# Performance work log

Hardware: AMD Instinct MI355X
Metric: run time of the kernel (lower is better)

The kernel has to match this reference:

```python
import jax, jax.numpy as jnp
import numpy as np

B, N, DIM = 8, 16384, 256
DIM_HEAD, NUM_HEADS = 64, 8
D = DIM_HEAD * NUM_HEADS  # 512
SCALE = DIM_HEAD ** (-0.5)


def setup_inputs() -> dict:
    key = jax.random.key(0)
    ks = jax.random.split(key, 11)
    s = 0.02
    return {
        "x": jax.random.normal(ks[0], (B, N, DIM), dtype=jnp.float32),
        "Wq": jax.random.normal(ks[1], (DIM, D), dtype=jnp.float32) * s,
        "bq": jax.random.normal(ks[2], (D,), dtype=jnp.float32) * s,
        "Wk": jax.random.normal(ks[3], (DIM, D), dtype=jnp.float32) * s,
        "bk": jax.random.normal(ks[4], (D,), dtype=jnp.float32) * s,
        "qw": jax.random.normal(ks[5], (D, 1), dtype=jnp.float32),  # query_weight parameter
        "Wp": jax.random.normal(ks[6], (D, D), dtype=jnp.float32) * s,
        "bp": jax.random.normal(ks[7], (D,), dtype=jnp.float32) * s,
        "Wo": jax.random.normal(ks[8], (D, DIM_HEAD), dtype=jnp.float32) * s,
        "bo": jax.random.normal(ks[9], (DIM_HEAD,), dtype=jnp.float32) * s,
    }


def reference(x, Wq, bq, Wk, bk, qw, Wp, bp, Wo, bo):
    # query, key: [B, N, D]
    query = jnp.einsum("bnc,cd->bnd", x, Wq) + bq
    key = jnp.einsum("bnc,cd->bnd", x, Wk) + bk
    # per-token scalar score: [B, N, 1]
    score = (query @ qw) * SCALE
    # global attention context: sum over sequence axis -> [B, 1, D]
    attn_weight = jnp.sum(score * query, axis=1, keepdims=True)
    # broadcast (repeat over N), gate keys, project, residual add of query
    out = jnp.einsum("bnd,de->bne", attn_weight * key, Wp) + bp + query
    # output projection D -> dim_head: [B, N, DIM_HEAD]
    out = jnp.einsum("bnd,dh->bnh", out, Wo) + bo
    return out
```

## Files before the change

kernel.cpp:

```cpp
#include <hip/hip_runtime.h>
#include <hip/hip_bf16.h>


#define NN 16384
#define CC 256
#define DD 512
#define HH 64
#define SCALE_F 0.125f

#define OFF_SX    0
#define OFF_TSUM  2048
#define OFF_WQQ   2056
#define OFF_BQQ   2312
#define OFF_WPWO  2320
#define OFF_WQWO  35088
#define OFF_CBIAS 51472
#define OFF_BEFF  51536
#define OFF_WEFFT 52048
#define OFF_AW    117584

typedef unsigned short ushort_t;
typedef __attribute__((ext_vector_type(8))) short short8;
typedef __attribute__((ext_vector_type(4))) float floatx4;

__device__ __forceinline__ unsigned short f2bf(float f) {
    __hip_bfloat16 h = __float2bfloat16(f);
    return __builtin_bit_cast(unsigned short, h);
}

__global__ __launch_bounds__(256) void k_prep(
    const float* __restrict__ Wq, const float* __restrict__ bq,
    const float* __restrict__ qw, const float* __restrict__ Wp,
    const float* __restrict__ bp, const float* __restrict__ Wo,
    const float* __restrict__ bo, float* __restrict__ ws)
{
    __shared__ float lds[2056];
    const int tid = threadIdx.x;
    const int bid = blockIdx.x;

    if (bid < 128) {
        const int d0 = bid * 4;
        for (int i = tid; i < 2048; i += 256) lds[i] = Wp[d0 * 512 + i];
        __syncthreads();
        const int dl = tid >> 6, h = tid & 63;
        float acc = 0.f;
        for (int e = 0; e < 512; ++e)
            acc = fmaf(lds[dl * 512 + e], Wo[e * 64 + h], acc);
        ws[OFF_WPWO + (d0 + dl) * 64 + h] = acc;
    } else if (bid < 192) {
        const int c0 = (bid - 128) * 4;
        for (int i = tid; i < 2048; i += 256) lds[i] = Wq[c0 * 512 + i];
        __syncthreads();
        const int cl = tid >> 6, h = tid & 63;
        float acc = 0.f;
        for (int e = 0; e < 512; ++e)
            acc = fmaf(lds[cl * 512 + e], Wo[e * 64 + h], acc);
        ws[OFF_WQWO + (c0 + cl) * 64 + h] = acc;
    } else if (bid == 192) {
        float* lb = lds + 2048;
        for (int i = tid; i < 512; i += 256) lds[i] = qw[i];
        if (tid == 0) *lb = 0.f;
        __syncthreads();
        const float* wr = Wq + tid * 512;
        float acc = 0.f;
        for (int d = 0; d < 512; ++d) acc = fmaf(wr[d], lds[d], acc);
        ws[OFF_WQQ + tid] = acc;
        float pb = fmaf(bq[tid], lds[tid], bq[tid + 256] * lds[tid + 256]);
#pragma unroll
        for (int m = 1; m < 64; m <<= 1) pb += __shfl_xor(pb, m);
        if ((tid & 63) == 0) atomicAdd(lb, pb);
        __syncthreads();
        if (tid == 0) ws[OFF_BQQ] = *lb;
    } else if (bid == 193) {
        const int h = tid & 63, part = tid >> 6;
        float acc = 0.f;
        for (int d = part * 128; d < part * 128 + 128; ++d)
            acc = fmaf(bq[d] + bp[d], Wo[d * 64 + h], acc);
        lds[part * 64 + h] = acc;
        __syncthreads();
        if (tid < 64)
            ws[OFF_CBIAS + tid] = bo[tid] + lds[tid] + lds[64 + tid] +
                                  lds[128 + tid] + lds[192 + tid];
    } else {
        for (int i = tid; i < 2056; i += 256) ws[OFF_SX + i] = 0.f;
    }
}

__global__ __launch_bounds__(256) void k_phase1(
    const float* __restrict__ x, float* __restrict__ ws)
{
    const int tid  = threadIdx.x;
    const int lane = tid & 63;
    const int wave = tid >> 6;
    const int quad = lane >> 4;
    const int l15  = lane & 15;
    __shared__ float lacc[256];
    __shared__ float ltsum;

    floatx4 wv[4];
#pragma unroll
    for (int j = 0; j < 4; ++j)
        wv[j] = *(const floatx4*)(ws + OFF_WQQ + j * 64 + l15 * 4);
    const float bqq = ws[OFF_BQQ];

    const int vb = blockIdx.x;
    const int b = vb >> 7;
    const int rbase = (vb & 127) * 128;
    lacc[tid] = 0.f;
    if (tid == 0) ltsum = 0.f;
    __syncthreads();

    const float* xb = x + (size_t)b * NN * CC;
    const int r0 = rbase + wave * 32 + quad;
    floatx4 accs[4];
#pragma unroll
    for (int j = 0; j < 4; ++j)
#pragma unroll
        for (int k = 0; k < 4; ++k) accs[j][k] = 0.f;
    float ts = 0.f;

#pragma unroll 2
    for (int it = 0; it < 8; ++it) {
        const float* xr = xb + (size_t)(r0 + it * 4) * CC + l15 * 4;
        const floatx4 x0 = *(const floatx4*)(xr);
        const floatx4 x1 = *(const floatx4*)(xr + 64);
        const floatx4 x2 = *(const floatx4*)(xr + 128);
        const floatx4 x3 = *(const floatx4*)(xr + 192);
        float p = 0.f;
#pragma unroll
        for (int k = 0; k < 4; ++k) {
            p = fmaf(x0[k], wv[0][k], p);
            p = fmaf(x1[k], wv[1][k], p);
            p = fmaf(x2[k], wv[2][k], p);
            p = fmaf(x3[k], wv[3][k], p);
        }
        p += __shfl_xor(p, 1);
        p += __shfl_xor(p, 2);
        p += __shfl_xor(p, 4);
        p += __shfl_xor(p, 8);
        const float t = SCALE_F * (p + bqq);
        ts += t;
#pragma unroll
        for (int k = 0; k < 4; ++k) {
            accs[0][k] = fmaf(t, x0[k], accs[0][k]);
            accs[1][k] = fmaf(t, x1[k], accs[1][k]);
            accs[2][k] = fmaf(t, x2[k], accs[2][k]);
            accs[3][k] = fmaf(t, x3[k], accs[3][k]);
        }
    }

#pragma unroll
    for (int j = 0; j < 4; ++j)
#pragma unroll
        for (int k = 0; k < 4; ++k) {
            float v = accs[j][k];
            v += __shfl_xor(v, 16);
            v += __shfl_xor(v, 32);
            if (quad == 0) atomicAdd(&lacc[j * 64 + l15 * 4 + k], v);
        }
    if (l15 == 0) atomicAdd(&ltsum, ts);
    __syncthreads();
    atomicAdd(&ws[OFF_SX + b * 256 + tid], lacc[tid]);
    if (tid == 0) atomicAdd(&ws[OFF_TSUM + b], ltsum);
}

__global__ __launch_bounds__(256) void k_aw(
    const float* __restrict__ Wq, const float* __restrict__ bq,
    float* __restrict__ ws)
{
    const int tid = threadIdx.x;
    const int b = blockIdx.y;
    const int d = blockIdx.x * 256 + tid;
    __shared__ float lsx[256];
    __shared__ float lts;
    lsx[tid] = ws[OFF_SX + b * 256 + tid];
    if (tid == 0) lts = ws[OFF_TSUM + b];
    __syncthreads();

    float a[8];
#pragma unroll
    for (int j = 0; j < 8; ++j) a[j] = 0.f;
    for (int c = 0; c < 256; c += 8) {
#pragma unroll
        for (int j = 0; j < 8; ++j)
            a[j] = fmaf(lsx[c + j], Wq[(c + j) * 512 + d], a[j]);
    }
    const float s = ((a[0] + a[1]) + (a[2] + a[3])) +
                    ((a[4] + a[5]) + (a[6] + a[7]));
    ws[OFF_AW + b * 512 + d] = lts * bq[d] + s;
}

__global__ __launch_bounds__(256) void k_weff(
    const float* __restrict__ Wk, const float* __restrict__ bk,
    float* __restrict__ ws)
{
    const int tid = threadIdx.x;
    const int b = blockIdx.y;
    const int c0 = blockIdx.x * 4;
    __shared__ float lred[256];

    const int cl = tid >> 6, h = tid & 63;
    const int c = c0 + cl;
    const float* law = ws + OFF_AW + (size_t)b * 512;
    const float* wkr = Wk + (size_t)c * 512;
    const float* wp  = ws + OFF_WPWO;

    float a0 = 0.f, a1 = 0.f, a2 = 0.f, a3 = 0.f;
    for (int d = 0; d < 512; d += 4) {
        a0 = fmaf(wkr[d + 0] * law[d + 0], wp[(d + 0) * 64 + h], a0);
        a1 = fmaf(wkr[d + 1] * law[d + 1], wp[(d + 1) * 64 + h], a1);
        a2 = fmaf(wkr[d + 2] * law[d + 2], wp[(d + 2) * 64 + h], a2);
        a3 = fmaf(wkr[d + 3] * law[d + 3], wp[(d + 3) * 64 + h], a3);
    }
    const float acc = ws[OFF_WQWO + c * 64 + h] + ((a0 + a1) + (a2 + a3));

    ushort_t* wt = (ushort_t*)(ws + OFF_WEFFT) + (size_t)b * (HH * CC);
    wt[(size_t)h * CC + c] = f2bf(acc);

    if (blockIdx.x == 0) {
        const int part = tid >> 6;
        float a = 0.f;
        for (int d = part * 128; d < part * 128 + 128; ++d)
            a = fmaf(bk[d] * law[d], wp[d * 64 + h], a);
        lred[tid] = a;
        __syncthreads();
        if (tid < 64)
            ws[OFF_BEFF + b * 64 + tid] = ws[OFF_CBIAS + tid] + lred[tid] +
                lred[64 + tid] + lred[128 + tid] + lred[192 + tid];
    }
}

__global__ __launch_bounds__(256) void k_out(
    const float* __restrict__ x, const float* __restrict__ ws,
    float* __restrict__ out)
{
    const int tid  = threadIdx.x;
    const int lane = tid & 63;
    const int wave = tid >> 6;
    const int quad = lane >> 4;
    const int l15  = lane & 15;
    __shared__ __align__(16) ushort_t lwt[64 * 264];

    const int vb = blockIdx.x;
    const int b = vb >> 7;
    const int rt0 = vb & 127;

    const int row0_0 = rt0 * 64 + wave * 16;
    const float* xr0 = x + ((size_t)b * NN + row0_0 + l15) * CC + quad * 8;
    short8 afrag0[8];
#pragma unroll
    for (int kk = 0; kk < 8; ++kk) {
        const floatx4 u0 = *(const floatx4*)(xr0 + kk * 32);
        const floatx4 u1 = *(const floatx4*)(xr0 + kk * 32 + 4);
        short8 t;
        t[0] = (short)f2bf(u0[0]); t[1] = (short)f2bf(u0[1]);
        t[2] = (short)f2bf(u0[2]); t[3] = (short)f2bf(u0[3]);
        t[4] = (short)f2bf(u1[0]); t[5] = (short)f2bf(u1[1]);
        t[6] = (short)f2bf(u1[2]); t[7] = (short)f2bf(u1[3]);
        afrag0[kk] = t;
    }

    const ushort_t* wt = (const ushort_t*)(ws + OFF_WEFFT) + (size_t)b * (HH * CC);
    for (int o = tid; o < 2048; o += 256) {
        const int h = o >> 5, seg = o & 31;
        *(short8*)(lwt + h * 264 + seg * 8) = *(const short8*)(wt + h * 256 + seg * 8);
    }
    __syncthreads();

    const float* beff = ws + OFF_BEFF + b * 64;
    float bias[4];
#pragma unroll
    for (int ht = 0; ht < 4; ++ht) bias[ht] = beff[ht * 16 + l15];

    {
        floatx4 acc[4];
#pragma unroll
        for (int ht = 0; ht < 4; ++ht)
#pragma unroll
            for (int r = 0; r < 4; ++r) acc[ht][r] = 0.f;
#pragma unroll
        for (int kk = 0; kk < 8; ++kk)
#pragma unroll
            for (int ht = 0; ht < 4; ++ht) {
                const short8 bf =
                    *(const short8*)(lwt + (ht * 16 + l15) * 264 + quad * 8 + kk * 32);
                acc[ht] = __builtin_amdgcn_mfma_f32_16x16x32_bf16(
                    afrag0[kk], bf, acc[ht], 0, 0, 0);
            }
#pragma unroll
        for (int ht = 0; ht < 4; ++ht) {
            const int h = ht * 16 + l15;
#pragma unroll
            for (int r = 0; r < 4; ++r) {
                const int row = row0_0 + quad * 4 + r;
                out[((size_t)b * NN + row) * HH + h] = acc[ht][r] + bias[ht];
            }
        }
    }

    {
        const int row0_1 = (rt0 + 128) * 64 + wave * 16;
        const float* xr1 = x + ((size_t)b * NN + row0_1 + l15) * CC + quad * 8;
        short8 afrag1[8];
#pragma unroll
        for (int kk = 0; kk < 8; ++kk) {
            const floatx4 u0 = *(const floatx4*)(xr1 + kk * 32);
            const floatx4 u1 = *(const floatx4*)(xr1 + kk * 32 + 4);
            short8 t;
            t[0] = (short)f2bf(u0[0]); t[1] = (short)f2bf(u0[1]);
            t[2] = (short)f2bf(u0[2]); t[3] = (short)f2bf(u0[3]);
            t[4] = (short)f2bf(u1[0]); t[5] = (short)f2bf(u1[1]);
            t[6] = (short)f2bf(u1[2]); t[7] = (short)f2bf(u1[3]);
            afrag1[kk] = t;
        }
        floatx4 acc[4];
#pragma unroll
        for (int ht = 0; ht < 4; ++ht)
#pragma unroll
            for (int r = 0; r < 4; ++r) acc[ht][r] = 0.f;
#pragma unroll
        for (int kk = 0; kk < 8; ++kk)
#pragma unroll
            for (int ht = 0; ht < 4; ++ht) {
                const short8 bf =
                    *(const short8*)(lwt + (ht * 16 + l15) * 264 + quad * 8 + kk * 32);
                acc[ht] = __builtin_amdgcn_mfma_f32_16x16x32_bf16(
                    afrag1[kk], bf, acc[ht], 0, 0, 0);
            }
#pragma unroll
        for (int ht = 0; ht < 4; ++ht) {
            const int h = ht * 16 + l15;
#pragma unroll
            for (int r = 0; r < 4; ++r) {
                const int row = row0_1 + quad * 4 + r;
                out[((size_t)b * NN + row) * HH + h] = acc[ht][r] + bias[ht];
            }
        }
    }
}

extern "C" void kernel_launch(void* const* d_in, const int* in_sizes, int n_in,
                              void* d_out, int out_size, void* d_ws, size_t ws_size,
                              hipStream_t stream) {
    const float* x  = (const float*)d_in[0];
    const float* Wq = (const float*)d_in[1];
    const float* bq = (const float*)d_in[2];
    const float* Wk = (const float*)d_in[3];
    const float* bk = (const float*)d_in[4];
    const float* qw = (const float*)d_in[5];
    const float* Wp = (const float*)d_in[6];
    const float* bp = (const float*)d_in[7];
    const float* Wo = (const float*)d_in[8];
    const float* bo = (const float*)d_in[9];
    float* ws  = (float*)d_ws;
    float* out = (float*)d_out;

    hipLaunchKernelGGL(k_prep,   dim3(195),    dim3(256), 0, stream,
                       Wq, bq, qw, Wp, bp, Wo, bo, ws);
    hipLaunchKernelGGL(k_phase1, dim3(1024),   dim3(256), 0, stream, x, ws);
    hipLaunchKernelGGL(k_aw,     dim3(2, 8),   dim3(256), 0, stream, Wq, bq, ws);
    hipLaunchKernelGGL(k_weff,   dim3(64, 8),  dim3(256), 0, stream, Wk, bk, ws);
    hipLaunchKernelGGL(k_out,    dim3(1024),   dim3(256), 0, stream, x, ws, out);
}
```

Baseline: 301.3 us.

## Split reductions across waves in small prep kernels to raise parallelism

The weight-folding kernels (prep, aw, weff) now split each dot-product reduction over four waves with an LDS reduction. Each block handles one output row instead of four, so the grids grow from 195/16/512 blocks to 770/64/2048. The goal is shorter serial reduction chains and more latency hiding in these small, latency-bound kernels. The cost is extra LDS reductions, barriers and more blocks launched; the main phase1 and out kernels are unchanged.

```diff
diff --git a/kernel.cpp b/kernel.cpp
--- a/kernel.cpp
+++ b/kernel.cpp
@@ -34,54 +34,61 @@
     const float* __restrict__ bp, const float* __restrict__ Wo,
     const float* __restrict__ bo, float* __restrict__ ws)
 {
-    __shared__ float lds[2056];
+    __shared__ float lds[520];
     const int tid = threadIdx.x;
     const int bid = blockIdx.x;
 
-    if (bid < 128) {
-        const int d0 = bid * 4;
-        for (int i = tid; i < 2048; i += 256) lds[i] = Wp[d0 * 512 + i];
-        __syncthreads();
-        const int dl = tid >> 6, h = tid & 63;
-        float acc = 0.f;
-        for (int e = 0; e < 512; ++e)
-            acc = fmaf(lds[dl * 512 + e], Wo[e * 64 + h], acc);
-        ws[OFF_WPWO + (d0 + dl) * 64 + h] = acc;
-    } else if (bid < 192) {
-        const int c0 = (bid - 128) * 4;
-        for (int i = tid; i < 2048; i += 256) lds[i] = Wq[c0 * 512 + i];
-        __syncthreads();
-        const int cl = tid >> 6, h = tid & 63;
-        float acc = 0.f;
-        for (int e = 0; e < 512; ++e)
-            acc = fmaf(lds[cl * 512 + e], Wo[e * 64 + h], acc);
-        ws[OFF_WQWO + (c0 + cl) * 64 + h] = acc;
-    } else if (bid == 192) {
-        float* lb = lds + 2048;
+    if (bid < 768) {
+        const bool is_wp = (bid < 512);
+        const int row = is_wp ? bid : (bid - 512);
+        const float* src = is_wp ? (Wp + (size_t)row * 512)
+                                 : (Wq + (size_t)row * 512);
+        const int h = tid & 63, part = tid >> 6;
+        const int e0 = part * 128;
+        float a0 = 0.f, a1 = 0.f, a2 = 0.f, a3 = 0.f;
+        for (int e = e0; e < e0 + 128; e += 4) {
+            a0 = fmaf(src[e + 0], Wo[(e + 0) * 64 + h], a0);
+            a1 = fmaf(src[e + 1], Wo[(e + 1) * 64 + h], a1);
+            a2 = fmaf(src[e + 2], Wo[(e + 2) * 64 + h], a2);
+            a3 = fmaf(src[e + 3], Wo[(e + 3) * 64 + h], a3);
+        }
+        lds[tid] = ((a0 + a1) + (a2 + a3));
+        __syncthreads();
+        if (tid < 64) {
+            const float v = lds[tid] + lds[64 + tid] + lds[128 + tid] + lds[192 + tid];
+            const int off = is_wp ? (OFF_WPWO + row * 64) : (OFF_WQWO + row * 64);
+            ws[off + tid] = v;
+        }
+    } else if (bid == 768) {
+        float* lb = lds + 512;
         for (int i = tid; i < 512; i += 256) lds[i] = qw[i];
         if (tid == 0) *lb = 0.f;
         __syncthreads();
-        const float* wr = Wq + tid * 512;
-        float acc = 0.f;
-        for (int d = 0; d < 512; ++d) acc = fmaf(wr[d], lds[d], acc);
-        ws[OFF_WQQ + tid] = acc;
+        const float* wr = Wq + (size_t)tid * 512;
+        float a0 = 0.f, a1 = 0.f, a2 = 0.f, a3 = 0.f;
+        for (int d = 0; d < 512; d += 4) {
+            a0 = fmaf(wr[d + 0], lds[d + 0], a0);
+            a1 = fmaf(wr[d + 1], lds[d + 1], a1);
+            a2 = fmaf(wr[d + 2], lds[d + 2], a2);
+            a3 = fmaf(wr[d + 3], lds[d + 3], a3);
+        }
+        ws[OFF_WQQ + tid] = ((a0 + a1) + (a2 + a3));
         float pb = fmaf(bq[tid], lds[tid], bq[tid + 256] * lds[tid + 256]);
 #pragma unroll
         for (int m = 1; m < 64; m <<= 1) pb += __shfl_xor(pb, m);
         if ((tid & 63) == 0) atomicAdd(lb, pb);
         __syncthreads();
         if (tid == 0) ws[OFF_BQQ] = *lb;
-    } else if (bid == 193) {
+    } else {
         const int h = tid & 63, part = tid >> 6;
         float acc = 0.f;
         for (int d = part * 128; d < part * 128 + 128; ++d)
             acc = fmaf(bq[d] + bp[d], Wo[d * 64 + h], acc);
-        lds[part * 64 + h] = acc;
+        lds[tid] = acc;
         __syncthreads();
         if (tid < 64)
             ws[OFF_CBIAS + tid] = bo[tid] + lds[tid] + lds[64 + tid] +
                                   lds[128 + tid] + lds[192 + tid];
-    } else {
         for (int i = tid; i < 2056; i += 256) ws[OFF_SX + i] = 0.f;
     }
 }
@@ -170,24 +177,30 @@
 {
     const int tid = threadIdx.x;
     const int b = blockIdx.y;
-    const int d = blockIdx.x * 256 + tid;
+    const int dl = tid & 63, part = tid >> 6;
+    const int d = blockIdx.x * 64 + dl;
     __shared__ float lsx[256];
+    __shared__ float lred[256];
     __shared__ float lts;
     lsx[tid] = ws[OFF_SX + b * 256 + tid];
     if (tid == 0) lts = ws[OFF_TSUM + b];
     __syncthreads();
 
-    float a[8];
-#pragma unroll
-    for (int j = 0; j < 8; ++j) a[j] = 0.f;
-    for (int c = 0; c < 256; c += 8) {
-#pragma unroll
-        for (int j = 0; j < 8; ++j)
-            a[j] = fmaf(lsx[c + j], Wq[(c + j) * 512 + d], a[j]);
-    }
-    const float s = ((a[0] + a[1]) + (a[2] + a[3])) +
-                    ((a[4] + a[5]) + (a[6] + a[7]));
-    ws[OFF_AW + b * 512 + d] = lts * bq[d] + s;
+    const int c0 = part * 64;
+    float a0 = 0.f, a1 = 0.f, a2 = 0.f, a3 = 0.f;
+    for (int c = c0; c < c0 + 64; c += 4) {
+        a0 = fmaf(lsx[c + 0], Wq[(c + 0) * 512 + d], a0);
+        a1 = fmaf(lsx[c + 1], Wq[(c + 1) * 512 + d], a1);
+        a2 = fmaf(lsx[c + 2], Wq[(c + 2) * 512 + d], a2);
+        a3 = fmaf(lsx[c + 3], Wq[(c + 3) * 512 + d], a3);
+    }
+    lred[tid] = ((a0 + a1) + (a2 + a3));
+    __syncthreads();
+    if (tid < 64) {
+        const float s = lred[tid] + lred[64 + tid] + lred[128 + tid] + lred[192 + tid];
+        const int dd = blockIdx.x * 64 + tid;
+        ws[OFF_AW + b * 512 + dd] = lts * bq[dd] + s;
+    }
 }
 
 __global__ __launch_bounds__(256) void k_weff(
@@ -196,31 +209,35 @@
 {
     const int tid = threadIdx.x;
     const int b = blockIdx.y;
-    const int c0 = blockIdx.x * 4;
+    const int c = blockIdx.x;
+    const int h = tid & 63, part = tid >> 6;
     __shared__ float lred[256];
 
-    const int cl = tid >> 6, h = tid & 63;
-    const int c = c0 + cl;
     const float* law = ws + OFF_AW + (size_t)b * 512;
     const float* wkr = Wk + (size_t)c * 512;
     const float* wp  = ws + OFF_WPWO;
 
+    const int d0 = part * 128;
     float a0 = 0.f, a1 = 0.f, a2 = 0.f, a3 = 0.f;
-    for (int d = 0; d < 512; d += 4) {
+    for (int d = d0; d < d0 + 128; d += 4) {
         a0 = fmaf(wkr[d + 0] * law[d + 0], wp[(d + 0) * 64 + h], a0);
         a1 = fmaf(wkr[d + 1] * law[d + 1], wp[(d + 1) * 64 + h], a1);
         a2 = fmaf(wkr[d + 2] * law[d + 2], wp[(d + 2) * 64 + h], a2);
         a3 = fmaf(wkr[d + 3] * law[d + 3], wp[(d + 3) * 64 + h], a3);
     }
-    const float acc = ws[OFF_WQWO + c * 64 + h] + ((a0 + a1) + (a2 + a3));
-
-    ushort_t* wt = (ushort_t*)(ws + OFF_WEFFT) + (size_t)b * (HH * CC);
-    wt[(size_t)h * CC + c] = f2bf(acc);
-
-    if (blockIdx.x == 0) {
-        const int part = tid >> 6;
+    lred[tid] = ((a0 + a1) + (a2 + a3));
+    __syncthreads();
+    if (tid < 64) {
+        const float v = ws[OFF_WQWO + c * 64 + tid] + lred[tid] +
+                        lred[64 + tid] + lred[128 + tid] + lred[192 + tid];
+        ushort_t* wt = (ushort_t*)(ws + OFF_WEFFT) + (size_t)b * (HH * CC);
+        wt[(size_t)tid * CC + c] = f2bf(v);
+    }
+
+    if (c == 0) {
+        __syncthreads();
         float a = 0.f;
-        for (int d = part * 128; d < part * 128 + 128; ++d)
+        for (int d = d0; d < d0 + 128; ++d)
             a = fmaf(bk[d] * law[d], wp[d * 64 + h], a);
         lred[tid] = a;
         __syncthreads();
@@ -355,10 +372,10 @@
     float* ws  = (float*)d_ws;
     float* out = (float*)d_out;
 
-    hipLaunchKernelGGL(k_prep,   dim3(195),    dim3(256), 0, stream,
+    hipLaunchKernelGGL(k_prep,   dim3(770),     dim3(256), 0, stream,
                        Wq, bq, qw, Wp, bp, Wo, bo, ws);
-    hipLaunchKernelGGL(k_phase1, dim3(1024),   dim3(256), 0, stream, x, ws);
-    hipLaunchKernelGGL(k_aw,     dim3(2, 8),   dim3(256), 0, stream, Wq, bq, ws);
-    hipLaunchKernelGGL(k_weff,   dim3(64, 8),  dim3(256), 0, stream, Wk, bk, ws);
-    hipLaunchKernelGGL(k_out,    dim3(1024),   dim3(256), 0, stream, x, ws, out);
-}
+    hipLaunchKernelGGL(k_phase1, dim3(1024),    dim3(256), 0, stream, x, ws);
+    hipLaunchKernelGGL(k_aw,     dim3(8, 8),    dim3(256), 0, stream, Wq, bq, ws);
+    hipLaunchKernelGGL(k_weff,   dim3(256, 8),  dim3(256), 0, stream, Wk, bk, ws);
+    hipLaunchKernelGGL(k_out,    dim3(1024),    dim3(256), 0, stream, x, ws, out);
+}
```

After: 311.9 us. 3.5% more time.
